# Kernel optimization log

Hardware: AMD Instinct MI355X
Metric: run time of the kernel (lower is better)

The kernel has to match this reference:

```python
import jax, jax.numpy as jnp
import numpy as np

D_MODEL = 1024
NUM_HEADS = 16
DEPTH = D_MODEL // NUM_HEADS


def setup_inputs() -> dict:
    key = jax.random.key(0)
    k_x, k_wqkv, k_bqkv, k_wp, k_bp = jax.random.split(key, 5)
    B, N = 2, 2048
    x = jax.random.normal(k_x, (B, N, D_MODEL), dtype=jnp.float32)
    scale = 1.0 / np.sqrt(D_MODEL)
    Wqkv = jax.random.normal(k_wqkv, (D_MODEL, 3 * D_MODEL), dtype=jnp.float32) * scale
    bqkv = jnp.zeros((3 * D_MODEL,), dtype=jnp.float32)
    Wproj = jax.random.normal(k_wp, (D_MODEL, D_MODEL), dtype=jnp.float32) * scale
    bproj = jnp.zeros((D_MODEL,), dtype=jnp.float32)
    return {"x": x, "Wqkv": Wqkv, "bqkv": bqkv, "Wproj": Wproj, "bproj": bproj}


def reference(x, Wqkv, bqkv, Wproj, bproj):
    B, N, C = x.shape
    # QKV projection; original layout: [B, N, H, depth, 3] -> transpose to [B, 3, H, N, depth]
    qkv = x @ Wqkv + bqkv                      # [B, N, 3C]
    qkv = qkv.reshape(B, N, NUM_HEADS, DEPTH, 3)
    qkv = jnp.transpose(qkv, (0, 4, 2, 1, 3))  # [B, 3, H, N, depth]
    q, k, v = qkv[:, 0], qkv[:, 1], qkv[:, 2]  # each [B, H, N, depth]
    # scaled dot-product attention (full N x N scores, as in the original)
    scale = 1.0 / jnp.sqrt(jnp.asarray(DEPTH, dtype=x.dtype))
    attn = jnp.einsum("bhnd,bhmd->bhnm", q, k) * scale
    attn = jax.nn.softmax(attn.astype(jnp.float32), axis=-1).astype(x.dtype)
    out = jnp.einsum("bhnm,bhmd->bhnd", attn, v)  # [B, H, N, depth]
    out = jnp.transpose(out, (0, 2, 1, 3)).reshape(B, N, C)
    return out @ Wproj + bproj
```

## Files before the change

### kernel.cpp

```cpp
#include <hip/hip_runtime.h>
#include <stdint.h>

#define D_MODEL 1024
#define NHEADS  16
#define DEPTH   64
#define BATCH   2
#define SEQ     2048
#define M_TOK   (BATCH*SEQ)

typedef __attribute__((ext_vector_type(8)))  short short8;
typedef __attribute__((ext_vector_type(4)))  float f32x4;
typedef __attribute__((ext_vector_type(16))) float f32x16;
typedef __attribute__((ext_vector_type(4)))  unsigned int uint4v;

#if defined(__has_builtin)
#if __has_builtin(__builtin_amdgcn_exp2f)
#define EXP2(x) __builtin_amdgcn_exp2f(x)
#endif
#endif
#ifndef EXP2
#define EXP2(x) exp2f(x)
#endif

__device__ __forceinline__ unsigned short f2bf(float f) {
  unsigned int u = __float_as_uint(f);
  u += 0x7fffu + ((u >> 16) & 1u);
  return (unsigned short)(u >> 16);
}

__device__ __forceinline__ unsigned int cvt_pk_bf16(float lo, float hi) {
  unsigned int r;
  asm("v_cvt_pk_bf16_f32 %0, %1, %2" : "=v"(r) : "v"(lo), "v"(hi));
  return r;
}

__device__ __forceinline__ void gload_lds16(const unsigned short* g, unsigned short* l) {
  __builtin_amdgcn_global_load_lds((const __attribute__((address_space(1))) void*)g,
                                   (__attribute__((address_space(3))) void*)l, 16, 0, 0);
}

__global__ void mha_prep(const float* __restrict__ x, const float* __restrict__ Wqkv,
                         const float* __restrict__ Wproj,
                         unsigned short* __restrict__ xb,
                         unsigned short* __restrict__ wqkT,
                         unsigned short* __restrict__ wvT,
                         unsigned short* __restrict__ wpT) {
  __shared__ float tile[32][33];
  int id = blockIdx.x, t = threadIdx.x;
  if (id < 2048) {
    int i = (id * 256 + t) * 8;
    float4 a = *(const float4*)(x + i);
    float4 b = *(const float4*)(x + i + 4);
    uint4 r;
    r.x = (unsigned)f2bf(a.x) | ((unsigned)f2bf(a.y) << 16);
    r.y = (unsigned)f2bf(a.z) | ((unsigned)f2bf(a.w) << 16);
    r.z = (unsigned)f2bf(b.x) | ((unsigned)f2bf(b.y) << 16);
    r.w = (unsigned)f2bf(b.z) | ((unsigned)f2bf(b.w) << 16);
    *(uint4*)(xb + i) = r;
  } else if (id < 5120) {
    int b = id - 2048;
    int c0 = (b % 96) * 32, k0 = (b / 96) * 32;
    int tx = t & 31, ty = t >> 5;
    for (int i = ty; i < 32; i += 8)
      tile[i][tx] = Wqkv[(size_t)(k0 + i) * 3072 + c0 + tx];
    __syncthreads();
    for (int i = ty; i < 32; i += 8) {
      int c = c0 + i;
      int hd = c / 3;
      int s = c - hd * 3;
      unsigned short v = f2bf(tile[tx][i]);
      if (s < 2) wqkT[(size_t)(s * 1024 + hd) * 1024 + k0 + tx] = v;
      else       wvT [(size_t)hd * 1024 + k0 + tx] = v;
    }
  } else {
    int b = id - 5120;
    int c0 = (b & 31) * 32, k0 = (b >> 5) * 32;
    int tx = t & 31, ty = t >> 5;
    for (int i = ty; i < 32; i += 8)
      tile[i][tx] = Wproj[(size_t)(k0 + i) * 1024 + c0 + tx];
    __syncthreads();
    for (int i = ty; i < 32; i += 8)
      wpT[(size_t)(c0 + i) * 1024 + k0 + tx] = f2bf(tile[tx][i]);
  }
}

__global__ __launch_bounds__(256, 3) void mha_gemm_qkv(
    const unsigned short* __restrict__ xb,
    const unsigned short* __restrict__ wqkT,
    const unsigned short* __restrict__ wvT,
    const float* __restrict__ bias,
    unsigned short* __restrict__ Qb,
    unsigned short* __restrict__ Kb,
    unsigned short* __restrict__ Vtb)
{
  __shared__ __align__(16) unsigned short As[128 * 64];
  __shared__ __align__(16) unsigned short Bs[128 * 64];
  const int K = 1024;
  int id = blockIdx.x;
  bool m0 = id < 512;
  int bx, by, bz = 0;
  const unsigned short *A, *Bt;
  if (m0) {
    int xcd = id & 7, idx = id >> 3;
    by = xcd * 4 + (idx >> 4);
    bx = idx & 15;
    A = xb; Bt = wqkT;
  } else {
    int b2 = id - 512;
    bx = b2 & 15; by = (b2 >> 4) & 7; bz = b2 >> 7;
    A = wvT; Bt = xb + (size_t)bz * SEQ * D_MODEL;
  }
  int t = threadIdx.x;
  int wv = t >> 6, lane = t & 63;
  int l15 = lane & 15, l4 = lane >> 4;
  int wr = wv >> 1, wc = wv & 1;
  int blkM = by * 128, blkN = bx * 128;

  f32x4 acc[4][4];
  for (int m = 0; m < 4; m++) for (int n = 0; n < 4; n++) acc[m][n] = (f32x4){0.f,0.f,0.f,0.f};

  for (int kt = 0; kt < K; kt += 64) {
    #pragma unroll
    for (int i = 0; i < 4; i++) {
      int e = i * 256 + t;
      int row = e >> 3;
      int sc = ((e & 7) ^ (row & 7)) * 8;
      gload_lds16(A  + (size_t)(blkM + row) * K + kt + sc, As + e * 8);
      gload_lds16(Bt + (size_t)(blkN + row) * K + kt + sc, Bs + e * 8);
    }
    __syncthreads();
    #pragma unroll
    for (int kk = 0; kk < 2; kk++) {
      int gp = ((kk * 4 + l4) ^ (l15 & 7)) * 8;
      short8 af[4], bf[4];
      #pragma unroll
      for (int m = 0; m < 4; m++)
        af[m] = *(const short8*)&As[(wr * 64 + m * 16 + l15) * 64 + gp];
      #pragma unroll
      for (int n = 0; n < 4; n++)
        bf[n] = *(const short8*)&Bs[(wc * 64 + n * 16 + l15) * 64 + gp];
      #pragma unroll
      for (int m = 0; m < 4; m++)
        #pragma unroll
        for (int n = 0; n < 4; n++)
          acc[m][n] = __builtin_amdgcn_mfma_f32_16x16x32_bf16(af[m], bf[n], acc[m][n], 0, 0, 0);
    }
    __syncthreads();
  }

  int row0 = blkM + wr * 64;
  int col0 = blkN + wc * 64;
  #pragma unroll
  for (int m = 0; m < 4; m++) {
    #pragma unroll
    for (int n = 0; n < 4; n++) {
      int colb = col0 + n * 16 + l15;
      #pragma unroll
      for (int j = 0; j < 4; j++) {
        int row = row0 + m * 16 + l4 * 4 + j;
        float v = acc[m][n][j];
        if (m0) {
          int s = colb >> 10, hd = colb & 1023;
          v += bias[hd * 3 + s];
          if (s == 0) v *= 0.18033688011112042f;
          size_t idx = ((size_t)((row >> 11) * NHEADS + (hd >> 6)) * SEQ + (row & 2047)) * DEPTH + (hd & 63);
          (s == 0 ? Qb : Kb)[idx] = f2bf(v);
        } else {
          v += bias[row * 3 + 2];
          Vtb[((size_t)(bz * 1024 + row)) * SEQ + colb] = f2bf(v);
        }
      }
    }
  }
}

__global__ __launch_bounds__(256, 3) void mha_gemm_proj(
    const unsigned short* __restrict__ A,
    const unsigned short* __restrict__ Bt,
    const float* __restrict__ bias,
    float* __restrict__ out_f)
{
  __shared__ __align__(16) unsigned short As[128 * 64];
  __shared__ __align__(16) unsigned short Bs[64 * 64];
  const int K = 1024;
  int id = blockIdx.x;
  int xcd = id & 7, idx = id >> 3;
  int by = xcd * 4 + (idx >> 4);
  int bx = idx & 15;
  int t = threadIdx.x;
  int wv = t >> 6, lane = t & 63;
  int l15 = lane & 15, l4 = lane >> 4;
  int wr = wv >> 1, wc = wv & 1;
  int blkM = by * 128, blkN = bx * 64;

  f32x4 acc[4][2];
  for (int m = 0; m < 4; m++) for (int n = 0; n < 2; n++) acc[m][n] = (f32x4){0.f,0.f,0.f,0.f};

  for (int kt = 0; kt < K; kt += 64) {
    #pragma unroll
    for (int i = 0; i < 4; i++) {
      int e = i * 256 + t;
      int row = e >> 3;
      int sc = ((e & 7) ^ (row & 7)) * 8;
      gload_lds16(A + (size_t)(blkM + row) * K + kt + sc, As + e * 8);
    }
    #pragma unroll
    for (int i = 0; i < 2; i++) {
      int e = i * 256 + t;
      int row = e >> 3;
      int sc = ((e & 7) ^ (row & 7)) * 8;
      gload_lds16(Bt + (size_t)(blkN + row) * K + kt + sc, Bs + e * 8);
    }
    __syncthreads();
    #pragma unroll
    for (int kk = 0; kk < 2; kk++) {
      int gp = ((kk * 4 + l4) ^ (l15 & 7)) * 8;
      short8 af[4], bf[2];
      #pragma unroll
      for (int m = 0; m < 4; m++)
        af[m] = *(const short8*)&As[(wr * 64 + m * 16 + l15) * 64 + gp];
      #pragma unroll
      for (int n = 0; n < 2; n++)
        bf[n] = *(const short8*)&Bs[(wc * 32 + n * 16 + l15) * 64 + gp];
      #pragma unroll
      for (int m = 0; m < 4; m++)
        #pragma unroll
        for (int n = 0; n < 2; n++)
          acc[m][n] = __builtin_amdgcn_mfma_f32_16x16x32_bf16(af[m], bf[n], acc[m][n], 0, 0, 0);
    }
    __syncthreads();
  }

  int row0 = blkM + wr * 64;
  int col0 = blkN + wc * 32;
  #pragma unroll
  for (int m = 0; m < 4; m++) {
    #pragma unroll
    for (int n = 0; n < 2; n++) {
      int colb = col0 + n * 16 + l15;
      #pragma unroll
      for (int j = 0; j < 4; j++) {
        int row = row0 + m * 16 + l4 * 4 + j;
        out_f[(size_t)row * D_MODEL + colb] = acc[m][n][j] + bias[colb];
      }
    }
  }
}

__global__ __launch_bounds__(512, 2) void mha_attn(
    const unsigned short* __restrict__ Q,
    const unsigned short* __restrict__ Kb,
    const unsigned short* __restrict__ Vt,
    unsigned short* __restrict__ O)
{
  const int N = SEQ;
  const int NIT = N / 64;
  int id = blockIdx.x;
  int bh    = (id & 7) * 4 + ((id >> 7) & 3);
  int qtile = (id >> 3) & 15;
  int t = threadIdx.x, wv = t >> 6, lane = t & 63;
  int l31 = lane & 31, hi = lane >> 5;
  int kh = wv & 1, qh = wv >> 1;

  __shared__ __align__(16) unsigned short SMEM[3 * 8192];

  const unsigned short* Kbh = Kb + (size_t)bh * N * DEPTH;
  const unsigned short* Vbh = Vt + (size_t)bh * DEPTH * N;

  int qrow = qtile * 128 + qh * 32 + l31;
  const unsigned short* Qp = Q + ((size_t)bh * N + qrow) * DEPTH + hi * 8;
  short8 qf[4];
  #pragma unroll
  for (int c = 0; c < 4; c++) qf[c] = *(const short8*)(Qp + c * 16);

  int srow = t >> 3;
  int sc8  = ((t & 7) ^ (srow & 7)) * 8;
  const unsigned short* kst = Kbh + (size_t)srow * DEPTH + sc8;
  const unsigned short* vst = Vbh + (size_t)srow * N + sc8;

  int rbK = (kh * 32 + l31) * 64;
  int rbV0 = l31 * 64, rbV1 = rbV0 + 2048;
  int goQK[4], goPV[2];
  #pragma unroll
  for (int c = 0; c < 4; c++) goQK[c] = ((c * 2 + hi) ^ (l31 & 7)) * 8;
  #pragma unroll
  for (int lc = 0; lc < 2; lc++) goPV[lc] = ((kh * 4 + lc * 2 + hi) ^ (l31 & 7)) * 8;

  short8 ones;
  #pragma unroll
  for (int i = 0; i < 8; i++) ones[i] = (short)0x3F80;

  f32x16 o0, o1, lsacc, zc;
  #pragma unroll
  for (int i = 0; i < 16; i++) { o0[i] = 0.f; o1[i] = 0.f; lsacc[i] = 0.f; zc[i] = 0.f; }

#define STAGE(buf, kt)                                                                  \
  do {                                                                                  \
    unsigned short* base = SMEM + (buf) * 8192;                                         \
    gload_lds16(kst + (size_t)(kt) * DEPTH, base + t * 8);                              \
    gload_lds16(vst + (kt),                 base + 4096 + t * 8);                       \
  } while (0)

  STAGE(0, 0);
  STAGE(1, 64);
  asm volatile("s_waitcnt vmcnt(2)" ::: "memory");
  __builtin_amdgcn_sched_barrier(0);
  __builtin_amdgcn_s_barrier();
  __builtin_amdgcn_sched_barrier(0);

  int cur = 0, sb = 2;
  for (int it = 0; it < NIT; ++it) {
    if (it + 2 < NIT) STAGE(sb, (it + 2) * 64);
    {
      const unsigned short* Kc = SMEM + cur * 8192;
      const unsigned short* Vc = Kc + 4096;
      __builtin_amdgcn_s_setprio(1);
      short8 ka0 = *(const short8*)&Kc[rbK + goQK[0]];
      f32x16 s = __builtin_amdgcn_mfma_f32_32x32x16_bf16(ka0, qf[0], zc, 0, 0, 0);
      #pragma unroll
      for (int c = 1; c < 4; c++) {
        short8 ka = *(const short8*)&Kc[rbK + goQK[c]];
        s = __builtin_amdgcn_mfma_f32_32x32x16_bf16(ka, qf[c], s, 0, 0, 0);
      }
      __builtin_amdgcn_s_setprio(0);
      float p[16];
      #pragma unroll
      for (int r = 0; r < 16; r++) p[r] = EXP2(s[r]);
      #pragma unroll
      for (int lc = 0; lc < 2; lc++) {
        unsigned int X0 = cvt_pk_bf16(p[8*lc+0], p[8*lc+1]);
        unsigned int X1 = cvt_pk_bf16(p[8*lc+2], p[8*lc+3]);
        unsigned int X2 = cvt_pk_bf16(p[8*lc+4], p[8*lc+5]);
        unsigned int X3 = cvt_pk_bf16(p[8*lc+6], p[8*lc+7]);
        auto r02 = __builtin_amdgcn_permlane32_swap(X0, X2, false, false);
        auto r13 = __builtin_amdgcn_permlane32_swap(X1, X3, false, false);
        uint4v wvec; wvec[0] = r02[0]; wvec[1] = r13[0]; wvec[2] = r02[1]; wvec[3] = r13[1];
        short8 bfrag = __builtin_bit_cast(short8, wvec);
        short8 va = *(const short8*)&Vc[rbV0 + goPV[lc]];
        short8 vb = *(const short8*)&Vc[rbV1 + goPV[lc]];
        __builtin_amdgcn_s_setprio(1);
        o0 = __builtin_amdgcn_mfma_f32_32x32x16_bf16(va, bfrag, o0, 0, 0, 0);
        o1 = __builtin_amdgcn_mfma_f32_32x32x16_bf16(vb, bfrag, o1, 0, 0, 0);
        lsacc = __builtin_amdgcn_mfma_f32_32x32x16_bf16(ones, bfrag, lsacc, 0, 0, 0);
        __builtin_amdgcn_s_setprio(0);
      }
    }
    if (it < NIT - 1) {
      if (it + 2 < NIT) asm volatile("s_waitcnt vmcnt(2)" ::: "memory");
      else              asm volatile("s_waitcnt vmcnt(0)" ::: "memory");
      __builtin_amdgcn_sched_barrier(0);
      __builtin_amdgcn_s_barrier();
      __builtin_amdgcn_sched_barrier(0);
    }
    cur = (cur == 2) ? 0 : cur + 1;
    sb  = (sb  == 2) ? 0 : sb  + 1;
  }
#undef STAGE

  float ls = lsacc[0];

  __syncthreads();
  float* cmb = (float*)SMEM;
  if (kh == 1) {
    float* c0 = cmb + (qh * 64 + lane) * 33;
    #pragma unroll
    for (int i = 0; i < 16; i++) { c0[i] = o0[i]; c0[16 + i] = o1[i]; }
    c0[32] = ls;
  }
  __syncthreads();
  if (kh == 0) {
    const float* c0 = cmb + (qh * 64 + lane) * 33;
    #pragma unroll
    for (int i = 0; i < 16; i++) { o0[i] += c0[i]; o1[i] += c0[16 + i]; }
    float rl = 1.0f / (ls + c0[32]);

    int b = bh >> 4, h = bh & 15;
    unsigned short* Op = O + ((size_t)b * N + qrow) * D_MODEL + h * DEPTH;
    #pragma unroll
    for (int gq = 0; gq < 4; gq++) {
      #pragma unroll
      for (int rp = 0; rp < 2; rp++) {
        int reg = gq * 4 + rp * 2;
        int d = gq * 8 + hi * 4 + rp * 2;
        *(unsigned int*)(Op + d)      = cvt_pk_bf16(o0[reg] * rl, o0[reg + 1] * rl);
        *(unsigned int*)(Op + 32 + d) = cvt_pk_bf16(o1[reg] * rl, o1[reg + 1] * rl);
      }
    }
  }
}

extern "C" void kernel_launch(void* const* d_in, const int* in_sizes, int n_in,
                              void* d_out, int out_size, void* d_ws, size_t ws_size,
                              hipStream_t stream) {
  const float* x     = (const float*)d_in[0];
  const float* Wqkv  = (const float*)d_in[1];
  const float* bqkv  = (const float*)d_in[2];
  const float* Wproj = (const float*)d_in[3];
  const float* bproj = (const float*)d_in[4];
  float* out = (float*)d_out;

  char* w = (char*)d_ws;
  unsigned short* xb    = (unsigned short*)(w);
  unsigned short* wqkT  = (unsigned short*)(w + 8388608);
  unsigned short* wvT   = (unsigned short*)(w + 8388608 + 4194304);
  unsigned short* wpT   = (unsigned short*)(w + 8388608 + 4194304 + 2097152);
  unsigned short* Qbuf  = (unsigned short*)(w + 16777216);
  unsigned short* Kbuf  = (unsigned short*)(w + 16777216 + 8388608);
  unsigned short* Vtb   = (unsigned short*)(w + 16777216 + 16777216);
  unsigned short* AOut  = (unsigned short*)(w + 16777216 + 25165824);

  mha_prep<<<6144, 256, 0, stream>>>(x, Wqkv, Wproj, xb, wqkT, wvT, wpT);
  mha_gemm_qkv<<<768, 256, 0, stream>>>(xb, wqkT, wvT, bqkv, Qbuf, Kbuf, Vtb);
  mha_attn<<<512, 512, 0, stream>>>(Qbuf, Kbuf, Vtb, AOut);
  mha_gemm_proj<<<512, 256, 0, stream>>>(AOut, wpT, bproj, out);
}
```

Baseline: 111.0 us.

## Software-pipeline QK MFMA one tile ahead and sum row totals on VALU

Restructures the attention inner loop so the QK^T MFMA for the next key tile is issued while exp/convert of the current tile and the PV MFMAs run, letting matrix and vector work overlap. The row-sum MFMA against a ones vector is replaced by scalar VALU accumulation of fp32 exponentials plus a cross-half shuffle, which removes one MFMA per chunk. The barrier now sits at the top of each iteration and waits with vmcnt(0), and the sum now uses unrounded fp32 values instead of bf16-rounded ones. Both changes add register pressure.

```diff
diff --git a/kernel.cpp b/kernel.cpp
--- a/kernel.cpp
+++ b/kernel.cpp
@@ -286,13 +286,10 @@
   #pragma unroll
   for (int lc = 0; lc < 2; lc++) goPV[lc] = ((kh * 4 + lc * 2 + hi) ^ (l31 & 7)) * 8;
 
-  short8 ones;
-  #pragma unroll
-  for (int i = 0; i < 8; i++) ones[i] = (short)0x3F80;
-
-  f32x16 o0, o1, lsacc, zc;
-  #pragma unroll
-  for (int i = 0; i < 16; i++) { o0[i] = 0.f; o1[i] = 0.f; lsacc[i] = 0.f; zc[i] = 0.f; }
+  f32x16 o0, o1, zc;
+  #pragma unroll
+  for (int i = 0; i < 16; i++) { o0[i] = 0.f; o1[i] = 0.f; zc[i] = 0.f; }
+  float ls0 = 0.f, ls1 = 0.f, ls2 = 0.f, ls3 = 0.f;
 
 #define STAGE(buf, kt)                                                                  \
   do {                                                                                  \
@@ -301,6 +298,19 @@
     gload_lds16(vst + (kt),                 base + 4096 + t * 8);                       \
   } while (0)
 
+#define QK_TILE(bufidx, sdst)                                                           \
+  do {                                                                                  \
+    const unsigned short* Kc = SMEM + (bufidx) * 8192;                                  \
+    __builtin_amdgcn_s_setprio(1);                                                      \
+    short8 ka0 = *(const short8*)&Kc[rbK + goQK[0]];                                    \
+    sdst = __builtin_amdgcn_mfma_f32_32x32x16_bf16(ka0, qf[0], zc, 0, 0, 0);            \
+    _Pragma("unroll") for (int c = 1; c < 4; c++) {                                     \
+      short8 ka = *(const short8*)&Kc[rbK + goQK[c]];                                   \
+      sdst = __builtin_amdgcn_mfma_f32_32x32x16_bf16(ka, qf[c], sdst, 0, 0, 0);         \
+    }                                                                                   \
+    __builtin_amdgcn_s_setprio(0);                                                      \
+  } while (0)
+
   STAGE(0, 0);
   STAGE(1, 64);
   asm volatile("s_waitcnt vmcnt(2)" ::: "memory");
@@ -308,56 +318,59 @@
   __builtin_amdgcn_s_barrier();
   __builtin_amdgcn_sched_barrier(0);
 
-  int cur = 0, sb = 2;
+  f32x16 s;
+  QK_TILE(0, s);
+
+  int cur = 0, nxt = 1, stg = 2;
   for (int it = 0; it < NIT; ++it) {
-    if (it + 2 < NIT) STAGE(sb, (it + 2) * 64);
+    asm volatile("s_waitcnt vmcnt(0)" ::: "memory");
+    __builtin_amdgcn_sched_barrier(0);
+    __builtin_amdgcn_s_barrier();
+    __builtin_amdgcn_sched_barrier(0);
+    if (it + 2 < NIT) STAGE(stg, (it + 2) * 64);
+
+    float p[16];
+    #pragma unroll
+    for (int r = 0; r < 16; r += 4) {
+      p[r]   = EXP2(s[r]);   ls0 += p[r];
+      p[r+1] = EXP2(s[r+1]); ls1 += p[r+1];
+      p[r+2] = EXP2(s[r+2]); ls2 += p[r+2];
+      p[r+3] = EXP2(s[r+3]); ls3 += p[r+3];
+    }
+    short8 bfA, bfB;
+    #pragma unroll
+    for (int lc = 0; lc < 2; lc++) {
+      unsigned int X0 = cvt_pk_bf16(p[8*lc+0], p[8*lc+1]);
+      unsigned int X1 = cvt_pk_bf16(p[8*lc+2], p[8*lc+3]);
+      unsigned int X2 = cvt_pk_bf16(p[8*lc+4], p[8*lc+5]);
+      unsigned int X3 = cvt_pk_bf16(p[8*lc+6], p[8*lc+7]);
+      auto r02 = __builtin_amdgcn_permlane32_swap(X0, X2, false, false);
+      auto r13 = __builtin_amdgcn_permlane32_swap(X1, X3, false, false);
+      uint4v wvec; wvec[0] = r02[0]; wvec[1] = r13[0]; wvec[2] = r02[1]; wvec[3] = r13[1];
+      if (lc == 0) bfA = __builtin_bit_cast(short8, wvec);
+      else         bfB = __builtin_bit_cast(short8, wvec);
+    }
+    if (it + 1 < NIT) QK_TILE(nxt, s);
     {
-      const unsigned short* Kc = SMEM + cur * 8192;
-      const unsigned short* Vc = Kc + 4096;
+      const unsigned short* Vc = SMEM + cur * 8192 + 4096;
+      short8 va0 = *(const short8*)&Vc[rbV0 + goPV[0]];
+      short8 vb0 = *(const short8*)&Vc[rbV1 + goPV[0]];
+      short8 va1 = *(const short8*)&Vc[rbV0 + goPV[1]];
+      short8 vb1 = *(const short8*)&Vc[rbV1 + goPV[1]];
       __builtin_amdgcn_s_setprio(1);
-      short8 ka0 = *(const short8*)&Kc[rbK + goQK[0]];
-      f32x16 s = __builtin_amdgcn_mfma_f32_32x32x16_bf16(ka0, qf[0], zc, 0, 0, 0);
-      #pragma unroll
-      for (int c = 1; c < 4; c++) {
-        short8 ka = *(const short8*)&Kc[rbK + goQK[c]];
-        s = __builtin_amdgcn_mfma_f32_32x32x16_bf16(ka, qf[c], s, 0, 0, 0);
-      }
+      o0 = __builtin_amdgcn_mfma_f32_32x32x16_bf16(va0, bfA, o0, 0, 0, 0);
+      o1 = __builtin_amdgcn_mfma_f32_32x32x16_bf16(vb0, bfA, o1, 0, 0, 0);
+      o0 = __builtin_amdgcn_mfma_f32_32x32x16_bf16(va1, bfB, o0, 0, 0, 0);
+      o1 = __builtin_amdgcn_mfma_f32_32x32x16_bf16(vb1, bfB, o1, 0, 0, 0);
       __builtin_amdgcn_s_setprio(0);
-      float p[16];
-      #pragma unroll
-      for (int r = 0; r < 16; r++) p[r] = EXP2(s[r]);
-      #pragma unroll
-      for (int lc = 0; lc < 2; lc++) {
-        unsigned int X0 = cvt_pk_bf16(p[8*lc+0], p[8*lc+1]);
-        unsigned int X1 = cvt_pk_bf16(p[8*lc+2], p[8*lc+3]);
-        unsigned int X2 = cvt_pk_bf16(p[8*lc+4], p[8*lc+5]);
-        unsigned int X3 = cvt_pk_bf16(p[8*lc+6], p[8*lc+7]);
-        auto r02 = __builtin_amdgcn_permlane32_swap(X0, X2, false, false);
-        auto r13 = __builtin_amdgcn_permlane32_swap(X1, X3, false, false);
-        uint4v wvec; wvec[0] = r02[0]; wvec[1] = r13[0]; wvec[2] = r02[1]; wvec[3] = r13[1];
-        short8 bfrag = __builtin_bit_cast(short8, wvec);
-        short8 va = *(const short8*)&Vc[rbV0 + goPV[lc]];
-        short8 vb = *(const short8*)&Vc[rbV1 + goPV[lc]];
-        __builtin_amdgcn_s_setprio(1);
-        o0 = __builtin_amdgcn_mfma_f32_32x32x16_bf16(va, bfrag, o0, 0, 0, 0);
-        o1 = __builtin_amdgcn_mfma_f32_32x32x16_bf16(vb, bfrag, o1, 0, 0, 0);
-        lsacc = __builtin_amdgcn_mfma_f32_32x32x16_bf16(ones, bfrag, lsacc, 0, 0, 0);
-        __builtin_amdgcn_s_setprio(0);
-      }
-    }
-    if (it < NIT - 1) {
-      if (it + 2 < NIT) asm volatile("s_waitcnt vmcnt(2)" ::: "memory");
-      else              asm volatile("s_waitcnt vmcnt(0)" ::: "memory");
-      __builtin_amdgcn_sched_barrier(0);
-      __builtin_amdgcn_s_barrier();
-      __builtin_amdgcn_sched_barrier(0);
-    }
-    cur = (cur == 2) ? 0 : cur + 1;
-    sb  = (sb  == 2) ? 0 : sb  + 1;
+    }
+    int oc = cur; cur = nxt; nxt = stg; stg = oc;
   }
 #undef STAGE
-
-  float ls = lsacc[0];
+#undef QK_TILE
+
+  float ls = (ls0 + ls1) + (ls2 + ls3);
+  ls += __shfl_xor(ls, 32);
 
   __syncthreads();
   float* cmb = (float*)SMEM;
```

After: 111.6 us. No clear change (+0.6%).

## Double-buffer LDS tiles in QKV and projection GEMMs with prefetch

Applied to the files above, without the earlier changes.

Both GEMM kernels now keep two LDS stages and issue the global-to-LDS loads for the next K tile before running the MFMAs on the current one. Each step ends with a single waitcnt and barrier instead of two barriers. This is meant to hide global load latency behind matrix math, and MFMA sections are given raised wave priority. The cost is twice the shared memory, so the QKV kernel's launch bounds drop from 3 to 2 blocks per CU, which lowers occupancy.

```diff
diff --git a/kernel.cpp b/kernel.cpp
--- a/kernel.cpp
+++ b/kernel.cpp
@@ -84,7 +84,7 @@
   }
 }
 
-__global__ __launch_bounds__(256, 3) void mha_gemm_qkv(
+__global__ __launch_bounds__(256, 2) void mha_gemm_qkv(
     const unsigned short* __restrict__ xb,
     const unsigned short* __restrict__ wqkT,
     const unsigned short* __restrict__ wvT,
@@ -93,8 +93,8 @@
     unsigned short* __restrict__ Kb,
     unsigned short* __restrict__ Vtb)
 {
-  __shared__ __align__(16) unsigned short As[128 * 64];
-  __shared__ __align__(16) unsigned short Bs[128 * 64];
+  __shared__ __align__(16) unsigned short As[2 * 128 * 64];
+  __shared__ __align__(16) unsigned short Bs[2 * 128 * 64];
   const int K = 1024;
   int id = blockIdx.x;
   bool m0 = id < 512;
@@ -119,34 +119,51 @@
   f32x4 acc[4][4];
   for (int m = 0; m < 4; m++) for (int n = 0; n < 4; n++) acc[m][n] = (f32x4){0.f,0.f,0.f,0.f};
 
-  for (int kt = 0; kt < K; kt += 64) {
-    #pragma unroll
-    for (int i = 0; i < 4; i++) {
-      int e = i * 256 + t;
-      int row = e >> 3;
-      int sc = ((e & 7) ^ (row & 7)) * 8;
-      gload_lds16(A  + (size_t)(blkM + row) * K + kt + sc, As + e * 8);
-      gload_lds16(Bt + (size_t)(blkN + row) * K + kt + sc, Bs + e * 8);
-    }
-    __syncthreads();
-    #pragma unroll
-    for (int kk = 0; kk < 2; kk++) {
-      int gp = ((kk * 4 + l4) ^ (l15 & 7)) * 8;
-      short8 af[4], bf[4];
-      #pragma unroll
-      for (int m = 0; m < 4; m++)
-        af[m] = *(const short8*)&As[(wr * 64 + m * 16 + l15) * 64 + gp];
-      #pragma unroll
-      for (int n = 0; n < 4; n++)
-        bf[n] = *(const short8*)&Bs[(wc * 64 + n * 16 + l15) * 64 + gp];
-      #pragma unroll
-      for (int m = 0; m < 4; m++)
-        #pragma unroll
-        for (int n = 0; n < 4; n++)
-          acc[m][n] = __builtin_amdgcn_mfma_f32_16x16x32_bf16(af[m], bf[n], acc[m][n], 0, 0, 0);
-    }
-    __syncthreads();
-  }
+#define GSTAGE(BUF, KT)                                                                 \
+  do {                                                                                  \
+    _Pragma("unroll") for (int i = 0; i < 4; i++) {                                     \
+      int e = i * 256 + t;                                                              \
+      int row = e >> 3;                                                                 \
+      int sc = ((e & 7) ^ (row & 7)) * 8;                                               \
+      gload_lds16(A  + (size_t)(blkM + row) * K + (KT) + sc, As + (BUF) * 8192 + e * 8);\
+      gload_lds16(Bt + (size_t)(blkN + row) * K + (KT) + sc, Bs + (BUF) * 8192 + e * 8);\
+    }                                                                                   \
+  } while (0)
+
+#define GBODY(BUF, KT)                                                                  \
+  do {                                                                                  \
+    if ((KT) + 64 < K) GSTAGE((BUF) ^ 1, (KT) + 64);                                    \
+    _Pragma("unroll") for (int kk = 0; kk < 2; kk++) {                                  \
+      int gp = ((kk * 4 + l4) ^ (l15 & 7)) * 8;                                         \
+      short8 af[4], bf[4];                                                              \
+      _Pragma("unroll") for (int m = 0; m < 4; m++)                                     \
+        af[m] = *(const short8*)&As[(BUF) * 8192 + (wr * 64 + m * 16 + l15) * 64 + gp]; \
+      _Pragma("unroll") for (int n = 0; n < 4; n++)                                     \
+        bf[n] = *(const short8*)&Bs[(BUF) * 8192 + (wc * 64 + n * 16 + l15) * 64 + gp]; \
+      __builtin_amdgcn_s_setprio(1);                                                    \
+      _Pragma("unroll") for (int m = 0; m < 4; m++)                                     \
+        _Pragma("unroll") for (int n = 0; n < 4; n++)                                   \
+          acc[m][n] = __builtin_amdgcn_mfma_f32_16x16x32_bf16(af[m], bf[n], acc[m][n], 0, 0, 0); \
+      __builtin_amdgcn_s_setprio(0);                                                    \
+    }                                                                                   \
+    asm volatile("s_waitcnt vmcnt(0)" ::: "memory");                                    \
+    __builtin_amdgcn_sched_barrier(0);                                                  \
+    __builtin_amdgcn_s_barrier();                                                       \
+    __builtin_amdgcn_sched_barrier(0);                                                  \
+  } while (0)
+
+  GSTAGE(0, 0);
+  asm volatile("s_waitcnt vmcnt(0)" ::: "memory");
+  __builtin_amdgcn_sched_barrier(0);
+  __builtin_amdgcn_s_barrier();
+  __builtin_amdgcn_sched_barrier(0);
+
+  for (int kt = 0; kt < K; kt += 128) {
+    GBODY(0, kt);
+    GBODY(1, kt + 64);
+  }
+#undef GSTAGE
+#undef GBODY
 
   int row0 = blkM + wr * 64;
   int col0 = blkN + wc * 64;
@@ -180,8 +197,8 @@
     const float* __restrict__ bias,
     float* __restrict__ out_f)
 {
-  __shared__ __align__(16) unsigned short As[128 * 64];
-  __shared__ __align__(16) unsigned short Bs[64 * 64];
+  __shared__ __align__(16) unsigned short As[2 * 128 * 64];
+  __shared__ __align__(16) unsigned short Bs[2 * 64 * 64];
   const int K = 1024;
   int id = blockIdx.x;
   int xcd = id & 7, idx = id >> 3;
@@ -196,40 +213,56 @@
   f32x4 acc[4][2];
   for (int m = 0; m < 4; m++) for (int n = 0; n < 2; n++) acc[m][n] = (f32x4){0.f,0.f,0.f,0.f};
 
-  for (int kt = 0; kt < K; kt += 64) {
-    #pragma unroll
-    for (int i = 0; i < 4; i++) {
-      int e = i * 256 + t;
-      int row = e >> 3;
-      int sc = ((e & 7) ^ (row & 7)) * 8;
-      gload_lds16(A + (size_t)(blkM + row) * K + kt + sc, As + e * 8);
-    }
-    #pragma unroll
-    for (int i = 0; i < 2; i++) {
-      int e = i * 256 + t;
-      int row = e >> 3;
-      int sc = ((e & 7) ^ (row & 7)) * 8;
-      gload_lds16(Bt + (size_t)(blkN + row) * K + kt + sc, Bs + e * 8);
-    }
-    __syncthreads();
-    #pragma unroll
-    for (int kk = 0; kk < 2; kk++) {
-      int gp = ((kk * 4 + l4) ^ (l15 & 7)) * 8;
-      short8 af[4], bf[2];
-      #pragma unroll
-      for (int m = 0; m < 4; m++)
-        af[m] = *(const short8*)&As[(wr * 64 + m * 16 + l15) * 64 + gp];
-      #pragma unroll
-      for (int n = 0; n < 2; n++)
-        bf[n] = *(const short8*)&Bs[(wc * 32 + n * 16 + l15) * 64 + gp];
-      #pragma unroll
-      for (int m = 0; m < 4; m++)
-        #pragma unroll
-        for (int n = 0; n < 2; n++)
-          acc[m][n] = __builtin_amdgcn_mfma_f32_16x16x32_bf16(af[m], bf[n], acc[m][n], 0, 0, 0);
-    }
-    __syncthreads();
-  }
+#define PSTAGE(BUF, KT)                                                                 \
+  do {                                                                                  \
+    _Pragma("unroll") for (int i = 0; i < 4; i++) {                                     \
+      int e = i * 256 + t;                                                              \
+      int row = e >> 3;                                                                 \
+      int sc = ((e & 7) ^ (row & 7)) * 8;                                               \
+      gload_lds16(A + (size_t)(blkM + row) * K + (KT) + sc, As + (BUF) * 8192 + e * 8); \
+    }                                                                                   \
+    _Pragma("unroll") for (int i = 0; i < 2; i++) {                                     \
+      int e = i * 256 + t;                                                              \
+      int row = e >> 3;                                                                 \
+      int sc = ((e & 7) ^ (row & 7)) * 8;                                               \
+      gload_lds16(Bt + (size_t)(blkN + row) * K + (KT) + sc, Bs + (BUF) * 4096 + e * 8);\
+    }                                                                                   \
+  } while (0)
+
+#define PBODY(BUF, KT)                                                                  \
+  do {                                                                                  \
+    if ((KT) + 64 < K) PSTAGE((BUF) ^ 1, (KT) + 64);                                    \
+    _Pragma("unroll") for (int kk = 0; kk < 2; kk++) {                                  \
+      int gp = ((kk * 4 + l4) ^ (l15 & 7)) * 8;                                         \
+      short8 af[4], bf[2];                                                              \
+      _Pragma("unroll") for (int m = 0; m < 4; m++)                                     \
+        af[m] = *(const short8*)&As[(BUF) * 8192 + (wr * 64 + m * 16 + l15) * 64 + gp]; \
+      _Pragma("unroll") for (int n = 0; n < 2; n++)                                     \
+        bf[n] = *(const short8*)&Bs[(BUF) * 4096 + (wc * 32 + n * 16 + l15) * 64 + gp]; \
+      __builtin_amdgcn_s_setprio(1);                                                    \
+      _Pragma("unroll") for (int m = 0; m < 4; m++)                                     \
+        _Pragma("unroll") for (int n = 0; n < 2; n++)                                   \
+          acc[m][n] = __builtin_amdgcn_mfma_f32_16x16x32_bf16(af[m], bf[n], acc[m][n], 0, 0, 0); \
+      __builtin_amdgcn_s_setprio(0);                                                    \
+    }                                                                                   \
+    asm volatile("s_waitcnt vmcnt(0)" ::: "memory");                                    \
+    __builtin_amdgcn_sched_barrier(0);                                                  \
+    __builtin_amdgcn_s_barrier();                                                       \
+    __builtin_amdgcn_sched_barrier(0);                                                  \
+  } while (0)
+
+  PSTAGE(0, 0);
+  asm volatile("s_waitcnt vmcnt(0)" ::: "memory");
+  __builtin_amdgcn_sched_barrier(0);
+  __builtin_amdgcn_s_barrier();
+  __builtin_amdgcn_sched_barrier(0);
+
+  for (int kt = 0; kt < K; kt += 128) {
+    PBODY(0, kt);
+    PBODY(1, kt + 64);
+  }
+#undef PSTAGE
+#undef PBODY
 
   int row0 = blkM + wr * 64;
   int col0 = blkN + wc * 32;
```

Measured after the change: 127.1 us. 1.15x slower.
